# Kernel optimization log

Measured on AMD Instinct MI355X. Metric: run time of the kernel, lower is better.

## Reference

```python
import jax, jax.numpy as jnp
import numpy as np

N_NODES = 100000
N_EDGES = 600000
FEAT = 128
N_RELS = 8


def setup_inputs() -> dict:
    key = jax.random.key(0)
    k1, k2, k3, k4, k5, k6, k7 = jax.random.split(key, 7)
    return {
        "h": jax.random.normal(k1, (N_NODES, FEAT), dtype=jnp.float32),
        "weight": jax.random.normal(k2, (N_RELS, FEAT, FEAT), dtype=jnp.float32) * (1.0 / np.sqrt(FEAT)),
        "gate_weight": jax.random.normal(k3, (N_RELS, FEAT, 1), dtype=jnp.float32) * (1.0 / np.sqrt(FEAT)),
        "norm": jax.random.uniform(k4, (N_EDGES, 1), dtype=jnp.float32),
        "src": jax.random.randint(k5, (N_EDGES,), 0, N_NODES, dtype=jnp.int32),
        "dst": jax.random.randint(k6, (N_EDGES,), 0, N_NODES, dtype=jnp.int32),
        "rel_type": jax.random.randint(k7, (N_EDGES,), 0, N_RELS, dtype=jnp.int32),
    }


def reference(h, weight, gate_weight, norm, src, dst, rel_type):
    # Transform every node by every relation once: [N, R, F].
    # Mathematically identical to per-edge bmm h_src @ W[rel], but avoids
    # materializing an [E, F, F] gathered weight tensor.
    h_all = jnp.einsum('nd,rdf->nrf', h, weight)            # [N, R, F]
    gate_all = jnp.einsum('nd,rdo->nro', h, gate_weight)[..., 0]  # [N, R]

    msg = h_all[src, rel_type] * norm                        # [E, F]
    gate = jax.nn.sigmoid(gate_all[src, rel_type])[:, None]  # [E, 1]
    msg = msg * gate

    out = jax.ops.segment_sum(msg, dst, num_segments=h.shape[0])  # scatter-sum to dst nodes
    return jax.nn.relu(out)
```

## Files before the change

### kernel.cpp

```cpp
#include <hip/hip_runtime.h>
#include <hip/hip_bf16.h>

#define FEAT 128
#define NRELS 8
#define KTOT 1024
#define BN 32
#define SCAN2 1024

typedef __bf16 bf16_t;
typedef __bf16 bf16x4_t __attribute__((ext_vector_type(4)));
typedef __bf16 bf16x8_t __attribute__((ext_vector_type(8)));
typedef float f32x4 __attribute__((ext_vector_type(4)));

struct __align__(8) PackedEdge { int row; float scale; };

static inline size_t align256(size_t x) { return (x + 255) & ~(size_t)255; }

__global__ void k_convert_w2(const float* __restrict__ w, bf16_t* __restrict__ wt2) {
    int i = blockIdx.x * blockDim.x + threadIdx.x;
    if (i >= NRELS * FEAT * FEAT) return;
    int r = i >> 14;
    int rem = i & 16383;
    int d = rem >> 7;
    int f = rem & 127;
    wt2[(size_t)f * KTOT + r * FEAT + d] = (bf16_t)w[i];
}

__global__ void k_convert_h(const float* __restrict__ h, bf16x4_t* __restrict__ hb4,
                            int ntotal) {
    int i = blockIdx.x * blockDim.x + threadIdx.x;
    if (i >= ntotal * (FEAT / 4)) return;
    float4 v = reinterpret_cast<const float4*>(h)[i];
    bf16x4_t o;
    o.x = (bf16_t)v.x; o.y = (bf16_t)v.y; o.z = (bf16_t)v.z; o.w = (bf16_t)v.w;
    hb4[i] = o;
}

__global__ __launch_bounds__(256) void k_gate(const float* __restrict__ h,
                                              const float* __restrict__ gw,
                                              float* __restrict__ sg, int ncount) {
    int wv = (int)((blockIdx.x * blockDim.x + threadIdx.x) >> 6);
    int lane = threadIdx.x & 63;
    if (wv >= ncount) return;
    int r = lane >> 3;
    int g = lane & 7;
    const float4* hp = reinterpret_cast<const float4*>(h + (size_t)wv * FEAT + g * 16);
    const float4* wp = reinterpret_cast<const float4*>(gw + r * FEAT + g * 16);
    float s = 0.f;
#pragma unroll
    for (int i = 0; i < 4; ++i) {
        float4 a = hp[i];
        float4 b = wp[i];
        s += a.x * b.x + a.y * b.y + a.z * b.z + a.w * b.w;
    }
    s += __shfl_xor(s, 1, 64);
    s += __shfl_xor(s, 2, 64);
    s += __shfl_xor(s, 4, 64);
    if (g == 0) sg[(size_t)wv * NRELS + r] = 1.0f / (1.0f + __expf(-s));
}

__global__ void k_degree8(const int* __restrict__ dstv, const int* __restrict__ rel,
                          int* __restrict__ deg8, int nedges) {
    int e = blockIdx.x * blockDim.x + threadIdx.x;
    if (e >= nedges) return;
    atomicAdd(&deg8[(dstv[e] << 3) | rel[e]], 1);
}

__global__ __launch_bounds__(1024) void k_scan_block2(const int* __restrict__ in,
                                                      int* __restrict__ outv,
                                                      int* __restrict__ bsum, int n) {
    __shared__ int sm[1024];
    int t = threadIdx.x;
    int idx = blockIdx.x * SCAN2 + t;
    int v = (idx < n) ? in[idx] : 0;
    sm[t] = v;
    __syncthreads();
    for (int off = 1; off < 1024; off <<= 1) {
        int x = (t >= off) ? sm[t - off] : 0;
        __syncthreads();
        sm[t] += x;
        __syncthreads();
    }
    if (idx < n) outv[idx] = sm[t] - v;
    if (t == 1023) bsum[blockIdx.x] = sm[1023];
}

__global__ __launch_bounds__(1024) void k_scan_tops(int* __restrict__ bsum, int nb,
                                                    int* __restrict__ rowptr_end) {
    __shared__ int sm[1024];
    int t = threadIdx.x;
    if (nb <= 1024) {
        int v = (t < nb) ? bsum[t] : 0;
        sm[t] = v;
        __syncthreads();
        for (int off = 1; off < 1024; off <<= 1) {
            int x = (t >= off) ? sm[t - off] : 0;
            __syncthreads();
            sm[t] += x;
            __syncthreads();
        }
        if (t < nb) bsum[t] = sm[t] - v;
        if (t == 1023) *rowptr_end = sm[1023];
    } else if (t == 0) {
        int run = 0;
        for (int b = 0; b < nb; ++b) { int v = bsum[b]; bsum[b] = run; run += v; }
        *rowptr_end = run;
    }
}

__global__ void k_scan_add2(int* __restrict__ rowptr, const int* __restrict__ bsum, int n) {
    int i = blockIdx.x * blockDim.x + threadIdx.x;
    if (i >= n) return;
    rowptr[i] += bsum[i >> 10];
}

__global__ void k_fill8(const int* __restrict__ src, const int* __restrict__ dstv,
                        const int* __restrict__ rel, const float* __restrict__ nrm,
                        const float* __restrict__ sg, const int* __restrict__ rp8,
                        int* __restrict__ cursor, PackedEdge* __restrict__ packed,
                        int nedges) {
    int e = blockIdx.x * blockDim.x + threadIdx.x;
    if (e >= nedges) return;
    int d = dstv[e];
    int s = src[e];
    int r = rel[e];
    int key = (d << 3) | r;
    int pos = rp8[key] + atomicAdd(&cursor[key], 1);
    PackedEdge p;
    p.row = (s << 3) | r;
    p.scale = nrm[e] * sg[(size_t)s * NRELS + r];
    packed[pos] = p;
}

__global__ __launch_bounds__(512, 2) void k_aggemm(const bf16_t* __restrict__ hb,
                                                   const bf16_t* __restrict__ wt2,
                                                   const PackedEdge* __restrict__ packed,
                                                   const int* __restrict__ rp8,
                                                   float* __restrict__ out, int nnodes) {
    __shared__ __align__(16) char lds_raw[BN * KTOT * sizeof(bf16_t)];
    float* cst = (float*)lds_raw;
    const int t = threadIdx.x;
    const int nb0 = blockIdx.x * BN;

    {
        f32x4 z = {0.f, 0.f, 0.f, 0.f};
#pragma unroll
        for (int i = 0; i < 8; ++i)
            reinterpret_cast<f32x4*>(lds_raw)[t + i * 512] = z;
    }
    __syncthreads();

    {
        const int g = t >> 4;
        const int il = t & 15;
        const int sw = g & 7;
        const int gnode = nb0 + g;
        int beg = 0, end = 0;
        if (gnode < nnodes) {
            beg = rp8[gnode * 8];
            end = rp8[gnode * 8 + 8];
        }
        float a[8];
#pragma unroll
        for (int i = 0; i < 8; ++i) a[i] = 0.f;

        int j = beg;
        PackedEdge p0 = {0, 0.f}, p1 = {0, 0.f};
        bf16x8_t v0;
#pragma unroll
        for (int i = 0; i < 8; ++i) v0[i] = (bf16_t)0.f;
        if (j < end) {
            p0 = packed[j];
            v0 = *reinterpret_cast<const bf16x8_t*>(
                hb + ((size_t)(p0.row >> 3) << 7) + il * 8);
        }
        if (j + 1 < end) p1 = packed[j + 1];
        int cur_r = (j < end) ? (p0.row & 7) : -1;

#pragma unroll 1
        for (; j < end; ++j) {
            bf16x8_t v1 = v0;
            if (j + 1 < end)
                v1 = *reinterpret_cast<const bf16x8_t*>(
                    hb + ((size_t)(p1.row >> 3) << 7) + il * 8);
            PackedEdge p2 = p1;
            if (j + 2 < end) p2 = packed[j + 2];
            int r = p0.row & 7;
            if (r != cur_r) {
                bf16x8_t o;
#pragma unroll
                for (int i = 0; i < 8; ++i) o[i] = (bf16_t)a[i];
                int chunk = (cur_r * 16 + il) ^ sw;
                *reinterpret_cast<bf16x8_t*>(lds_raw + (size_t)g * 2048 + chunk * 16) = o;
#pragma unroll
                for (int i = 0; i < 8; ++i) a[i] = 0.f;
                cur_r = r;
            }
            float s = p0.scale;
#pragma unroll
            for (int i = 0; i < 8; ++i) a[i] += (float)v0[i] * s;
            p0 = p1; p1 = p2; v0 = v1;
        }
        if (cur_r >= 0) {
            bf16x8_t o;
#pragma unroll
            for (int i = 0; i < 8; ++i) o[i] = (bf16_t)a[i];
            int chunk = (cur_r * 16 + il) ^ sw;
            *reinterpret_cast<bf16x8_t*>(lds_raw + (size_t)g * 2048 + chunk * 16) = o;
        }
    }
    __syncthreads();

    const int lane = t & 63;
    const int wv = t >> 6;
    const int l15 = lane & 15;
    const int lhi = lane >> 4;
    f32x4 acc0 = {0.f, 0.f, 0.f, 0.f};
    f32x4 acc1 = {0.f, 0.f, 0.f, 0.f};
    const bf16_t* bp = wt2 + (size_t)(wv * 16 + l15) * KTOT + lhi * 8;
    const char* a0p = lds_raw + (size_t)l15 * 2048;
    const char* a1p = a0p + 16 * 2048;
    const int sw = l15 & 7;
#pragma unroll 4
    for (int ks = 0; ks < 32; ++ks) {
        int coff = ((ks * 4 + lhi) ^ sw) << 4;
        bf16x8_t av0 = *reinterpret_cast<const bf16x8_t*>(a0p + coff);
        bf16x8_t av1 = *reinterpret_cast<const bf16x8_t*>(a1p + coff);
        bf16x8_t bv = *reinterpret_cast<const bf16x8_t*>(bp + ks * 32);
        acc0 = __builtin_amdgcn_mfma_f32_16x16x32_bf16(av0, bv, acc0, 0, 0, 0);
        acc1 = __builtin_amdgcn_mfma_f32_16x16x32_bf16(av1, bv, acc1, 0, 0, 0);
    }
    __syncthreads();

    {
        int f = wv * 16 + l15;
#pragma unroll
        for (int i = 0; i < 4; ++i) {
            int n0 = lhi * 4 + i;
            cst[n0 * 132 + f] = acc0[i];
            cst[(n0 + 16) * 132 + f] = acc1[i];
        }
    }
    __syncthreads();

    {
        int node = t >> 4;
        int f0 = (t & 15) * 8;
        int gnode = nb0 + node;
        if (gnode < nnodes) {
            const float* cr = cst + node * 132 + f0;
            float4 o0, o1;
            o0.x = fmaxf(cr[0], 0.f); o0.y = fmaxf(cr[1], 0.f);
            o0.z = fmaxf(cr[2], 0.f); o0.w = fmaxf(cr[3], 0.f);
            o1.x = fmaxf(cr[4], 0.f); o1.y = fmaxf(cr[5], 0.f);
            o1.z = fmaxf(cr[6], 0.f); o1.w = fmaxf(cr[7], 0.f);
            float4* op = reinterpret_cast<float4*>(out + (size_t)gnode * FEAT + f0);
            op[0] = o0;
            op[1] = o1;
        }
    }
}

extern "C" void kernel_launch(void* const* d_in, const int* in_sizes, int n_in,
                              void* d_out, int out_size, void* d_ws, size_t ws_size,
                              hipStream_t stream) {
    const float* h = (const float*)d_in[0];
    const float* w = (const float*)d_in[1];
    const float* gw = (const float*)d_in[2];
    const float* nrm = (const float*)d_in[3];
    const int* src = (const int*)d_in[4];
    const int* dst = (const int*)d_in[5];
    const int* rel = (const int*)d_in[6];
    float* out = (float*)d_out;

    const int N = in_sizes[0] / FEAT;
    const int E = in_sizes[4];
    const int NSEG = N * NRELS;
    const int nb2 = (NSEG + SCAN2 - 1) / SCAN2;
    const int nbk = (N + BN - 1) / BN;

    char* ws = (char*)d_ws;
    const size_t wt2B = align256((size_t)FEAT * KTOT * sizeof(bf16_t));
    const size_t hbB  = align256((size_t)N * FEAT * sizeof(bf16_t));
    const size_t sgB  = align256((size_t)N * NRELS * sizeof(float));
    const size_t dgB  = align256((size_t)NSEG * sizeof(int));
    const size_t rpB  = align256((size_t)(NSEG + 1) * sizeof(int));
    const size_t bsB  = align256((size_t)nb2 * sizeof(int));

    bf16_t* wt2 = (bf16_t*)ws;
    bf16_t* hb = (bf16_t*)(ws + wt2B);
    float* sg = (float*)(ws + wt2B + hbB);
    int* deg8 = (int*)(ws + wt2B + hbB + sgB);
    int* rp8 = (int*)(ws + wt2B + hbB + sgB + dgB);
    int* bsum = (int*)(ws + wt2B + hbB + sgB + dgB + rpB);
    PackedEdge* packed = (PackedEdge*)(ws + wt2B + hbB + sgB + dgB + rpB + bsB);

    k_convert_w2<<<(NRELS * FEAT * FEAT + 255) / 256, 256, 0, stream>>>(w, wt2);
    k_convert_h<<<(N * (FEAT / 4) + 255) / 256, 256, 0, stream>>>(h, (bf16x4_t*)hb, N);
    k_gate<<<(N + 3) / 4, 256, 0, stream>>>(h, gw, sg, N);

    hipMemsetAsync(deg8, 0, (size_t)NSEG * sizeof(int), stream);
    k_degree8<<<(E + 255) / 256, 256, 0, stream>>>(dst, rel, deg8, E);
    k_scan_block2<<<nb2, 1024, 0, stream>>>(deg8, rp8, bsum, NSEG);
    k_scan_tops<<<1, 1024, 0, stream>>>(bsum, nb2, rp8 + NSEG);
    k_scan_add2<<<(NSEG + 255) / 256, 256, 0, stream>>>(rp8, bsum, NSEG);
    hipMemsetAsync(deg8, 0, (size_t)NSEG * sizeof(int), stream);
    k_fill8<<<(E + 255) / 256, 256, 0, stream>>>(src, dst, rel, nrm, sg, rp8, deg8,
                                                 packed, E);

    k_aggemm<<<nbk, 512, 0, stream>>>(hb, wt2, packed, rp8, out, N);
}
```

Baseline: 366.0 us.

## Fuse h conversion into gate kernel, reuse scan output as fill cursor, deepen gather prefetch

Three independent changes. The bf16 conversion of h is merged into the gate kernel, which removes one launch and a second read of h. The scan-add kernel now writes the final row pointers into a cursor array, so the fill kernel can use a single atomicAdd directly and no longer needs a memset or an extra rp8 read. The edge-gather loop in k_aggemm is restructured to process four edges per iteration, with packed-edge loads prefetched eight ahead and row loads four ahead, to expose more memory-level parallelism. Launch bounds are raised to four blocks per CU, which risks register pressure or spills given the deeper prefetch state.

```diff
diff --git a/kernel.cpp b/kernel.cpp
--- a/kernel.cpp
+++ b/kernel.cpp
@@ -8,6 +8,7 @@
 #define SCAN2 1024
 
 typedef __bf16 bf16_t;
+typedef __bf16 bf16x2_t __attribute__((ext_vector_type(2)));
 typedef __bf16 bf16x4_t __attribute__((ext_vector_type(4)));
 typedef __bf16 bf16x8_t __attribute__((ext_vector_type(8)));
 typedef float f32x4 __attribute__((ext_vector_type(4)));
@@ -26,22 +27,20 @@
     wt2[(size_t)f * KTOT + r * FEAT + d] = (bf16_t)w[i];
 }
 
-__global__ void k_convert_h(const float* __restrict__ h, bf16x4_t* __restrict__ hb4,
-                            int ntotal) {
-    int i = blockIdx.x * blockDim.x + threadIdx.x;
-    if (i >= ntotal * (FEAT / 4)) return;
-    float4 v = reinterpret_cast<const float4*>(h)[i];
-    bf16x4_t o;
-    o.x = (bf16_t)v.x; o.y = (bf16_t)v.y; o.z = (bf16_t)v.z; o.w = (bf16_t)v.w;
-    hb4[i] = o;
-}
-
-__global__ __launch_bounds__(256) void k_gate(const float* __restrict__ h,
+__global__ __launch_bounds__(256) void k_prep(const float* __restrict__ h,
                                               const float* __restrict__ gw,
-                                              float* __restrict__ sg, int ncount) {
+                                              float* __restrict__ sg,
+                                              bf16_t* __restrict__ hb, int ncount) {
     int wv = (int)((blockIdx.x * blockDim.x + threadIdx.x) >> 6);
     int lane = threadIdx.x & 63;
     if (wv >= ncount) return;
+
+    float2 hv2 = *reinterpret_cast<const float2*>(h + (size_t)wv * FEAT + lane * 2);
+    bf16x2_t hc;
+    hc.x = (bf16_t)hv2.x;
+    hc.y = (bf16_t)hv2.y;
+    *reinterpret_cast<bf16x2_t*>(hb + (size_t)wv * FEAT + lane * 2) = hc;
+
     int r = lane >> 3;
     int g = lane & 7;
     const float4* hp = reinterpret_cast<const float4*>(h + (size_t)wv * FEAT + g * 16);
@@ -108,31 +107,32 @@
     }
 }
 
-__global__ void k_scan_add2(int* __restrict__ rowptr, const int* __restrict__ bsum, int n) {
+__global__ void k_scan_add2(int* __restrict__ rowptr, const int* __restrict__ bsum,
+                            int* __restrict__ wcur, int n) {
     int i = blockIdx.x * blockDim.x + threadIdx.x;
     if (i >= n) return;
-    rowptr[i] += bsum[i >> 10];
+    int v = rowptr[i] + bsum[i >> 10];
+    rowptr[i] = v;
+    wcur[i] = v;
 }
 
 __global__ void k_fill8(const int* __restrict__ src, const int* __restrict__ dstv,
                         const int* __restrict__ rel, const float* __restrict__ nrm,
-                        const float* __restrict__ sg, const int* __restrict__ rp8,
-                        int* __restrict__ cursor, PackedEdge* __restrict__ packed,
-                        int nedges) {
+                        const float* __restrict__ sg, int* __restrict__ wcur,
+                        PackedEdge* __restrict__ packed, int nedges) {
     int e = blockIdx.x * blockDim.x + threadIdx.x;
     if (e >= nedges) return;
     int d = dstv[e];
     int s = src[e];
     int r = rel[e];
-    int key = (d << 3) | r;
-    int pos = rp8[key] + atomicAdd(&cursor[key], 1);
+    int pos = atomicAdd(&wcur[(d << 3) | r], 1);
     PackedEdge p;
     p.row = (s << 3) | r;
     p.scale = nrm[e] * sg[(size_t)s * NRELS + r];
     packed[pos] = p;
 }
 
-__global__ __launch_bounds__(512, 2) void k_aggemm(const bf16_t* __restrict__ hb,
+__global__ __launch_bounds__(512, 4) void k_aggemm(const bf16_t* __restrict__ hb,
                                                    const bf16_t* __restrict__ wt2,
                                                    const PackedEdge* __restrict__ packed,
                                                    const int* __restrict__ rp8,
@@ -160,53 +160,73 @@
             beg = rp8[gnode * 8];
             end = rp8[gnode * 8 + 8];
         }
-        float a[8];
-#pragma unroll
-        for (int i = 0; i < 8; ++i) a[i] = 0.f;
-
-        int j = beg;
-        PackedEdge p0 = {0, 0.f}, p1 = {0, 0.f};
-        bf16x8_t v0;
-#pragma unroll
-        for (int i = 0; i < 8; ++i) v0[i] = (bf16_t)0.f;
-        if (j < end) {
+
+        if (beg < end) {
+            float a[8];
+#pragma unroll
+            for (int i = 0; i < 8; ++i) a[i] = 0.f;
+            int cur_r;
+
+            auto ldrow = [&](const PackedEdge& p) {
+                return *reinterpret_cast<const bf16x8_t*>(
+                    hb + ((size_t)(p.row >> 3) << 7) + il * 8);
+            };
+            auto flush = [&](int rr) {
+                bf16x8_t o;
+#pragma unroll
+                for (int i = 0; i < 8; ++i) o[i] = (bf16_t)a[i];
+                int chunk = (rr * 16 + il) ^ sw;
+                *reinterpret_cast<bf16x8_t*>(lds_raw + (size_t)g * 2048 + chunk * 16) = o;
+            };
+            auto consume = [&](const PackedEdge& p, const bf16x8_t& v, int idx) {
+                if (idx < end) {
+                    int r = p.row & 7;
+                    if (r != cur_r) {
+                        flush(cur_r);
+#pragma unroll
+                        for (int i = 0; i < 8; ++i) a[i] = 0.f;
+                        cur_r = r;
+                    }
+                    float s = p.scale;
+#pragma unroll
+                    for (int i = 0; i < 8; ++i) a[i] += (float)v[i] * s;
+                }
+            };
+
+            int j = beg;
+            PackedEdge p0, p1, p2, p3, q0, q1, q2, q3;
             p0 = packed[j];
-            v0 = *reinterpret_cast<const bf16x8_t*>(
-                hb + ((size_t)(p0.row >> 3) << 7) + il * 8);
-        }
-        if (j + 1 < end) p1 = packed[j + 1];
-        int cur_r = (j < end) ? (p0.row & 7) : -1;
+            p1 = (j + 1 < end) ? packed[j + 1] : p0;
+            p2 = (j + 2 < end) ? packed[j + 2] : p0;
+            p3 = (j + 3 < end) ? packed[j + 3] : p0;
+            q0 = (j + 4 < end) ? packed[j + 4] : p0;
+            q1 = (j + 5 < end) ? packed[j + 5] : p0;
+            q2 = (j + 6 < end) ? packed[j + 6] : p0;
+            q3 = (j + 7 < end) ? packed[j + 7] : p0;
+            bf16x8_t v0 = ldrow(p0);
+            bf16x8_t v1 = ldrow(p1);
+            bf16x8_t v2 = ldrow(p2);
+            bf16x8_t v3 = ldrow(p3);
+            cur_r = p0.row & 7;
 
 #pragma unroll 1
-        for (; j < end; ++j) {
-            bf16x8_t v1 = v0;
-            if (j + 1 < end)
-                v1 = *reinterpret_cast<const bf16x8_t*>(
-                    hb + ((size_t)(p1.row >> 3) << 7) + il * 8);
-            PackedEdge p2 = p1;
-            if (j + 2 < end) p2 = packed[j + 2];
-            int r = p0.row & 7;
-            if (r != cur_r) {
-                bf16x8_t o;
-#pragma unroll
-                for (int i = 0; i < 8; ++i) o[i] = (bf16_t)a[i];
-                int chunk = (cur_r * 16 + il) ^ sw;
-                *reinterpret_cast<bf16x8_t*>(lds_raw + (size_t)g * 2048 + chunk * 16) = o;
-#pragma unroll
-                for (int i = 0; i < 8; ++i) a[i] = 0.f;
-                cur_r = r;
+            for (; j < end; j += 4) {
+                PackedEdge r0 = p0, r1 = p0, r2 = p0, r3 = p0;
+                if (j + 8 < end)  r0 = packed[j + 8];
+                if (j + 9 < end)  r1 = packed[j + 9];
+                if (j + 10 < end) r2 = packed[j + 10];
+                if (j + 11 < end) r3 = packed[j + 11];
+
+                consume(p0, v0, j);
+                consume(p1, v1, j + 1);
+                consume(p2, v2, j + 2);
+                consume(p3, v3, j + 3);
+
+                v0 = ldrow(q0); v1 = ldrow(q1); v2 = ldrow(q2); v3 = ldrow(q3);
+                p0 = q0; p1 = q1; p2 = q2; p3 = q3;
+                q0 = r0; q1 = r1; q2 = r2; q3 = r3;
             }
-            float s = p0.scale;
-#pragma unroll
-            for (int i = 0; i < 8; ++i) a[i] += (float)v0[i] * s;
-            p0 = p1; p1 = p2; v0 = v1;
-        }
-        if (cur_r >= 0) {
-            bf16x8_t o;
-#pragma unroll
-            for (int i = 0; i < 8; ++i) o[i] = (bf16_t)a[i];
-            int chunk = (cur_r * 16 + il) ^ sw;
-            *reinterpret_cast<bf16x8_t*>(lds_raw + (size_t)g * 2048 + chunk * 16) = o;
+            flush(cur_r);
         }
     }
     __syncthreads();
@@ -296,16 +316,14 @@
     PackedEdge* packed = (PackedEdge*)(ws + wt2B + hbB + sgB + dgB + rpB + bsB);
 
     k_convert_w2<<<(NRELS * FEAT * FEAT + 255) / 256, 256, 0, stream>>>(w, wt2);
-    k_convert_h<<<(N * (FEAT / 4) + 255) / 256, 256, 0, stream>>>(h, (bf16x4_t*)hb, N);
-    k_gate<<<(N + 3) / 4, 256, 0, stream>>>(h, gw, sg, N);
+    k_prep<<<(N + 3) / 4, 256, 0, stream>>>(h, gw, sg, hb, N);
 
     hipMemsetAsync(deg8, 0, (size_t)NSEG * sizeof(int), stream);
     k_degree8<<<(E + 255) / 256, 256, 0, stream>>>(dst, rel, deg8, E);
     k_scan_block2<<<nb2, 1024, 0, stream>>>(deg8, rp8, bsum, NSEG);
     k_scan_tops<<<1, 1024, 0, stream>>>(bsum, nb2, rp8 + NSEG);
-    k_scan_add2<<<(NSEG + 255) / 256, 256, 0, stream>>>(rp8, bsum, NSEG);
-    hipMemsetAsync(deg8, 0, (size_t)NSEG * sizeof(int), stream);
-    k_fill8<<<(E + 255) / 256, 256, 0, stream>>>(src, dst, rel, nrm, sg, rp8, deg8,
+    k_scan_add2<<<(NSEG + 255) / 256, 256, 0, stream>>>(rp8, bsum, deg8, NSEG);
+    k_fill8<<<(E + 255) / 256, 256, 0, stream>>>(src, dst, rel, nrm, sg, deg8,
                                                  packed, E);
 
     k_aggemm<<<nbk, 512, 0, stream>>>(hb, wt2, packed, rp8, out, N);
```

Result: faster. 346.6 us (-5.3%).
